# Kernel optimization log

Hardware: AMD Instinct MI355X
Metric: run time of the kernel (lower is better)

Reference implementation:

```python
import jax, jax.numpy as jnp
import numpy as np

# fp4 e2m1 representable magnitudes and round-to-nearest midpoints
_FP4_LEVELS = jnp.array([0.0, 0.5, 1.0, 1.5, 2.0, 3.0, 4.0, 6.0], dtype=jnp.float32)
_FP4_MIDS = jnp.array([0.25, 0.75, 1.25, 1.75, 2.5, 3.5, 5.0], dtype=jnp.float32)


def fp4_get_scalar(x):
    return jnp.mean(jnp.abs(x))


def fp4_quant_dequant(x, s):
    # quant(x, s) then rquant(x, s): round x/s to nearest fp4e2m1 value, scale back
    y = x / s
    idx = jnp.searchsorted(_FP4_MIDS, jnp.abs(y), side='right')
    q = jnp.sign(y) * _FP4_LEVELS[idx]
    return q * s


def setup_inputs() -> dict:
    key = jax.random.key(0)
    k1, k2, k3 = jax.random.split(key, 3)
    B, S, IN, OUT = 4, 2048, 4096, 4096
    input = jax.random.normal(k1, (B, S, IN), dtype=jnp.float32)
    # kaiming-uniform-ish weight, small bias
    bound_w = np.sqrt(6.0 / IN) / np.sqrt(1 + 5.0)
    weight = jax.random.uniform(k2, (OUT, IN), minval=-bound_w, maxval=bound_w, dtype=jnp.float32)
    bound_b = 1.0 / np.sqrt(IN)
    bias = jax.random.uniform(k3, (OUT,), minval=-bound_b, maxval=bound_b, dtype=jnp.float32)
    return {"input": input, "weight": weight, "bias": bias}


def reference(input, weight, bias):
    q_scalar = 1.0
    input_scalar = fp4_get_scalar(input) * q_scalar
    weight_scalar = fp4_get_scalar(weight) * q_scalar
    x_q = fp4_quant_dequant(input, input_scalar)      # [B,S,IN]
    w_q = fp4_quant_dequant(weight, weight_scalar)    # [OUT,IN]
    out = jnp.einsum('bsi,oi->bso', x_q, w_q) + bias  # [B,S,OUT]
    return out
```

## Files before the change

### kernel.cpp

```cpp
#include <hip/hip_runtime.h>
#include <hip/hip_bf16.h>
#include <stdint.h>

typedef __attribute__((ext_vector_type(16))) float f32x16;
typedef __attribute__((ext_vector_type(8))) int i32x8;

#define M_DIM 8192
#define N_DIM 4096
#define K_DIM 4096
#define NX_INV (1.0f / 33554432.0f)
#define NW_INV (1.0f / 16777216.0f)

#define AS3(p) ((__attribute__((address_space(3))) uint32_t*)(uint32_t)(uintptr_t)(p))
#define AS1(p) ((const __attribute__((address_space(1))) uint32_t*)(uintptr_t)(p))

__global__ void absum2_kernel(const float* __restrict__ x, const float* __restrict__ w,
                              double* __restrict__ sums) {
    bool isw = blockIdx.x >= 2048;
    const float4* src = (const float4*)(isw ? w : x);
    int n4  = isw ? (16777216 / 4) : (33554432 / 4);
    int bid = isw ? (blockIdx.x - 2048) : blockIdx.x;
    int nb  = isw ? 1024 : 2048;
    int i = bid * blockDim.x + threadIdx.x;
    int stride = nb * blockDim.x;
    float s = 0.f;
    for (; i < n4; i += stride) {
        float4 v = src[i];
        s += fabsf(v.x) + fabsf(v.y) + fabsf(v.z) + fabsf(v.w);
    }
    #pragma unroll
    for (int off = 32; off >= 1; off >>= 1) s += __shfl_down(s, off, 64);
    __shared__ float wsum[4];
    int lane = threadIdx.x & 63, wid = threadIdx.x >> 6;
    if (lane == 0) wsum[wid] = s;
    __syncthreads();
    if (threadIdx.x == 0) {
        double tot = (double)wsum[0] + (double)wsum[1] + (double)wsum[2] + (double)wsum[3];
        atomicAdd(&sums[isw ? 1 : 0], tot);
    }
}

__device__ __forceinline__ uint32_t enc_nib_t(float x, float t0, float t1, float t2,
                                              float t3, float t4, float t5, float t6) {
    float a = fabsf(x);
    uint32_t idx;
    if (a < t3) idx = (a < t1) ? ((a < t0) ? 0u : 1u) : ((a < t2) ? 2u : 3u);
    else        idx = (a < t5) ? ((a < t4) ? 4u : 5u) : ((a < t6) ? 6u : 7u);
    return idx | ((__float_as_uint(x) >> 31) << 3);
}

__global__ void quant2_kernel(const float* __restrict__ X, const float* __restrict__ W,
                              uint32_t* __restrict__ Xp, uint32_t* __restrict__ Wp,
                              const double* __restrict__ sums) {
    __shared__ float4 tile[32 * 64];

    bool isw = blockIdx.x >= 4096;
    const float* src_base = isw ? W : X;
    uint32_t* dst = isw ? Wp : Xp;
    float s = (float)(sums[isw ? 1 : 0]) * (isw ? NW_INV : NX_INV);
    int bid = isw ? (blockIdx.x - 4096) : blockIdx.x;

    float t0 = 0.25f * s, t1 = 0.75f * s, t2 = 1.25f * s, t3 = 1.75f * s;
    float t4 = 2.5f * s,  t5 = 3.5f * s,  t6 = 5.0f * s;

    int mb  = bid >> 4;
    int ktg = bid & 15;
    int t = threadIdx.x;

    {
        int row0 = t >> 6;
        int col4 = t & 63;
        const float4* src = (const float4*)(src_base + (size_t)(mb * 32 + row0) * K_DIM + ktg * 256) + col4;
        #pragma unroll
        for (int p = 0; p < 8; p++) {
            int row = p * 4 + row0;
            tile[row * 64 + (col4 ^ (row & 7))] = src[(size_t)p * 4 * (K_DIM / 4)];
        }
    }
    __syncthreads();

    int w = t >> 6;
    int l = t & 63;
    int row = l & 31;
    int ub = w * 16 + (l >> 5) * 8;
    uint32_t o[4];
    #pragma unroll
    for (int d = 0; d < 4; d++) {
        float4 f0 = tile[row * 64 + ((ub + 2 * d)     ^ (row & 7))];
        float4 f1 = tile[row * 64 + ((ub + 2 * d + 1) ^ (row & 7))];
        o[d] =  enc_nib_t(f0.x, t0,t1,t2,t3,t4,t5,t6)
             | (enc_nib_t(f0.y, t0,t1,t2,t3,t4,t5,t6) << 4)
             | (enc_nib_t(f0.z, t0,t1,t2,t3,t4,t5,t6) << 8)
             | (enc_nib_t(f0.w, t0,t1,t2,t3,t4,t5,t6) << 12)
             | (enc_nib_t(f1.x, t0,t1,t2,t3,t4,t5,t6) << 16)
             | (enc_nib_t(f1.y, t0,t1,t2,t3,t4,t5,t6) << 20)
             | (enc_nib_t(f1.z, t0,t1,t2,t3,t4,t5,t6) << 24)
             | (enc_nib_t(f1.w, t0,t1,t2,t3,t4,t5,t6) << 28);
    }
    int kt = ktg * 4 + w;
    *(uint4*)(dst + ((size_t)(mb * 64 + kt) * 64 + l) * 4) = make_uint4(o[0], o[1], o[2], o[3]);
}

#define NWG 512

__device__ __forceinline__ void glds16(const uint32_t* g, uint32_t* l) {
    __builtin_amdgcn_global_load_lds(AS1(g), AS3(l), 16, 0, 0);
}

__device__ __forceinline__ i32x8 dupfrag(uint4 u) {
    i32x8 v;
    v[0] = u.x; v[1] = u.y; v[2] = u.z; v[3] = u.w;
    v[4] = u.x; v[5] = u.y; v[6] = u.z; v[7] = u.w;
    return v;
}

#define MFMA2(VA, C0, C1) do {                                                    \
    i32x8 va_ = dupfrag(VA);                                                      \
    C0 = __builtin_amdgcn_mfma_scale_f32_32x32x64_f8f6f4(va_, vb0_, C0, 4, 4, 0, 0x7F7F7F7F, 0, 0x7F7F7F7F); \
    C1 = __builtin_amdgcn_mfma_scale_f32_32x32x64_f8f6f4(va_, vb1_, C1, 4, 4, 0, 0x7F7F7F7F, 0, 0x7F7F7F7F); \
} while (0)

#define EPI(ACC, MM, NN) do {                                                     \
    int col_ = colb + (NN) * 32;                                                  \
    float bv_ = bias[col_];                                                       \
    _Pragma("unroll")                                                             \
    for (int i = 0; i < 16; i++) {                                                \
        int row_ = rowb + (MM) * 32 + (i & 3) + ((i >> 2) << 3);                  \
        __builtin_nontemporal_store(ACC[i] * scale + bv_,                         \
                                    &C[(size_t)row_ * N_DIM + col_]);             \
    }                                                                             \
} while (0)

__global__ __launch_bounds__(512, 2)
void gemm_kernel(const uint32_t* __restrict__ Ap, const uint32_t* __restrict__ Bp,
                 const float* __restrict__ bias, float* __restrict__ C,
                 const double* __restrict__ sums) {
    __shared__ uint32_t lds[4 * 4096];

    int bid = blockIdx.x;
    int swz = (bid & 7) * 64 + (bid >> 3);
    int bm = (swz >> 4) * 256;
    int bn = (swz & 15) * 256;

    int t = threadIdx.x;
    int lane = t & 63;
    int wid = t >> 6;
    int wm = wid >> 2;
    int wn = wid & 3;

    const uint32_t* gA = Ap + (size_t)((bm >> 5) + (t >> 6)) * 16384 + (t & 63) * 4;
    const uint32_t* gB = Bp + (size_t)((bn >> 5) + (t >> 6)) * 16384 + (t & 63) * 4;
    uint32_t* ldA = lds + t * 4;
    uint32_t* ldB = lds + 2048 + t * 4;

    int oA0 = ((wm * 4 + 0) * 64 + lane) * 4;
    int oA1 = ((wm * 4 + 1) * 64 + lane) * 4;
    int oA2 = ((wm * 4 + 2) * 64 + lane) * 4;
    int oA3 = ((wm * 4 + 3) * 64 + lane) * 4;
    int oB0 = 2048 + ((wn * 2 + 0) * 64 + lane) * 4;
    int oB1 = 2048 + ((wn * 2 + 1) * 64 + lane) * 4;

    f32x16 acc00 = (f32x16)0.f, acc01 = (f32x16)0.f;
    f32x16 acc10 = (f32x16)0.f, acc11 = (f32x16)0.f;
    f32x16 acc20 = (f32x16)0.f, acc21 = (f32x16)0.f;
    f32x16 acc30 = (f32x16)0.f, acc31 = (f32x16)0.f;

    glds16(gA + 0,   ldA + 0);
    glds16(gB + 0,   ldB + 0);
    glds16(gA + 256, ldA + 4096);
    glds16(gB + 256, ldB + 4096);

    for (int kt = 0; kt < 64; kt++) {
        if (kt < 63) asm volatile("s_waitcnt vmcnt(2)" ::: "memory");
        else         asm volatile("s_waitcnt vmcnt(0)" ::: "memory");
        __builtin_amdgcn_s_barrier();

        const uint32_t* rb = lds + (kt & 3) * 4096;
        int so = ((kt + 2) & 3) * 4096;

        if (kt < 62) glds16(gA + (kt + 2) * 256, ldA + so);
        uint4 rA0 = *(const uint4*)&rb[oA0];
        uint4 rA1 = *(const uint4*)&rb[oA1];
        uint4 rB0 = *(const uint4*)&rb[oB0];
        uint4 rB1 = *(const uint4*)&rb[oB1];
        i32x8 vb0_ = dupfrag(rB0);
        i32x8 vb1_ = dupfrag(rB1);
        __builtin_amdgcn_s_setprio(1);
        MFMA2(rA0, acc00, acc01);
        MFMA2(rA1, acc10, acc11);
        __builtin_amdgcn_s_setprio(0);
        __builtin_amdgcn_s_barrier();

        if (kt < 62) glds16(gB + (kt + 2) * 256, ldB + so);
        uint4 rA2 = *(const uint4*)&rb[oA2];
        uint4 rA3 = *(const uint4*)&rb[oA3];
        __builtin_amdgcn_s_setprio(1);
        MFMA2(rA2, acc20, acc21);
        MFMA2(rA3, acc30, acc31);
        __builtin_amdgcn_s_setprio(0);
    }

    float scale = (float)((sums[0] * (1.0 / 33554432.0)) * (sums[1] * (1.0 / 16777216.0)));

    int colb = bn + wn * 64 + (lane & 31);
    int rowb = bm + wm * 128 + ((lane >> 5) << 2);
    EPI(acc00, 0, 0); EPI(acc01, 0, 1);
    EPI(acc10, 1, 0); EPI(acc11, 1, 1);
    EPI(acc20, 2, 0); EPI(acc21, 2, 1);
    EPI(acc30, 3, 0); EPI(acc31, 3, 1);
}

extern "C" void kernel_launch(void* const* d_in, const int* in_sizes, int n_in,
                              void* d_out, int out_size, void* d_ws, size_t ws_size,
                              hipStream_t stream) {
    const float* x    = (const float*)d_in[0];
    const float* w    = (const float*)d_in[1];
    const float* bias = (const float*)d_in[2];
    float* out = (float*)d_out;

    double* sums = (double*)d_ws;
    uint32_t* Xp = (uint32_t*)((char*)d_ws + 1024);
    uint32_t* Wp = Xp + (size_t)256 * 64 * 64 * 4;

    hipMemsetAsync(d_ws, 0, 1024, stream);
    absum2_kernel<<<3072, 256, 0, stream>>>(x, w, sums);
    quant2_kernel<<<6144, 256, 0, stream>>>(x, w, Xp, Wp, sums);
    gemm_kernel<<<NWG, 512, 0, stream>>>(Xp, Wp, bias, out, sums);
}
```

Baseline: 220.3 us.

## Load B fragments directly to registers, stage only A through LDS

Each wave now loads its B operand fragments straight from global memory into registers with a two-stage register double buffer, instead of staging B through LDS. Only A goes through LDS, which halves shared memory use and removes the second barrier per k-step, and the loop is unrolled by two. The cost is that the B tile is loaded redundantly by each wave row (two wm groups), so global/L2 traffic for B rises, and the vmcnt wait logic now has to account for the extra register loads.

```diff
diff --git a/kernel.cpp b/kernel.cpp
--- a/kernel.cpp
+++ b/kernel.cpp
@@ -120,6 +120,30 @@
     C1 = __builtin_amdgcn_mfma_scale_f32_32x32x64_f8f6f4(va_, vb1_, C1, 4, 4, 0, 0x7F7F7F7F, 0, 0x7F7F7F7F); \
 } while (0)
 
+#define STEP(S, KT) do {                                                          \
+    if ((KT) < 63) asm volatile("s_waitcnt vmcnt(3)" ::: "memory");               \
+    else           asm volatile("s_waitcnt vmcnt(0)" ::: "memory");               \
+    __builtin_amdgcn_s_barrier();                                                 \
+    const uint32_t* rb_ = lds + (((KT) & 3) << 11);                               \
+    i32x8 vb0_ = dupfrag(S##b0);                                                  \
+    i32x8 vb1_ = dupfrag(S##b1);                                                  \
+    if ((KT) + 2 < 64) {                                                          \
+        glds16(gA + ((KT) + 2) * 256, lds + ((((KT) + 2) & 3) << 11) + t * 4);    \
+        S##b0 = *(const uint4*)(pB0 + (size_t)((KT) + 2) * 256);                  \
+        S##b1 = *(const uint4*)(pB1 + (size_t)((KT) + 2) * 256);                  \
+    }                                                                             \
+    uint4 rA0_ = *(const uint4*)&rb_[oA0];                                        \
+    uint4 rA1_ = *(const uint4*)&rb_[oA1];                                        \
+    uint4 rA2_ = *(const uint4*)&rb_[oA2];                                        \
+    uint4 rA3_ = *(const uint4*)&rb_[oA3];                                        \
+    __builtin_amdgcn_s_setprio(1);                                                \
+    MFMA2(rA0_, acc00, acc01);                                                    \
+    MFMA2(rA1_, acc10, acc11);                                                    \
+    MFMA2(rA2_, acc20, acc21);                                                    \
+    MFMA2(rA3_, acc30, acc31);                                                    \
+    __builtin_amdgcn_s_setprio(0);                                                \
+} while (0)
+
 #define EPI(ACC, MM, NN) do {                                                     \
     int col_ = colb + (NN) * 32;                                                  \
     float bv_ = bias[col_];                                                       \
@@ -135,7 +159,7 @@
 void gemm_kernel(const uint32_t* __restrict__ Ap, const uint32_t* __restrict__ Bp,
                  const float* __restrict__ bias, float* __restrict__ C,
                  const double* __restrict__ sums) {
-    __shared__ uint32_t lds[4 * 4096];
+    __shared__ uint32_t lds[4 * 2048];
 
     int bid = blockIdx.x;
     int swz = (bid & 7) * 64 + (bid >> 3);
@@ -149,55 +173,32 @@
     int wn = wid & 3;
 
     const uint32_t* gA = Ap + (size_t)((bm >> 5) + (t >> 6)) * 16384 + (t & 63) * 4;
-    const uint32_t* gB = Bp + (size_t)((bn >> 5) + (t >> 6)) * 16384 + (t & 63) * 4;
-    uint32_t* ldA = lds + t * 4;
-    uint32_t* ldB = lds + 2048 + t * 4;
+
+    const uint32_t* pB0 = Bp + (size_t)((bn >> 5) + wn * 2 + 0) * 16384 + lane * 4;
+    const uint32_t* pB1 = Bp + (size_t)((bn >> 5) + wn * 2 + 1) * 16384 + lane * 4;
 
     int oA0 = ((wm * 4 + 0) * 64 + lane) * 4;
     int oA1 = ((wm * 4 + 1) * 64 + lane) * 4;
     int oA2 = ((wm * 4 + 2) * 64 + lane) * 4;
     int oA3 = ((wm * 4 + 3) * 64 + lane) * 4;
-    int oB0 = 2048 + ((wn * 2 + 0) * 64 + lane) * 4;
-    int oB1 = 2048 + ((wn * 2 + 1) * 64 + lane) * 4;
 
     f32x16 acc00 = (f32x16)0.f, acc01 = (f32x16)0.f;
     f32x16 acc10 = (f32x16)0.f, acc11 = (f32x16)0.f;
     f32x16 acc20 = (f32x16)0.f, acc21 = (f32x16)0.f;
     f32x16 acc30 = (f32x16)0.f, acc31 = (f32x16)0.f;
 
-    glds16(gA + 0,   ldA + 0);
-    glds16(gB + 0,   ldB + 0);
-    glds16(gA + 256, ldA + 4096);
-    glds16(gB + 256, ldB + 4096);
-
-    for (int kt = 0; kt < 64; kt++) {
-        if (kt < 63) asm volatile("s_waitcnt vmcnt(2)" ::: "memory");
-        else         asm volatile("s_waitcnt vmcnt(0)" ::: "memory");
-        __builtin_amdgcn_s_barrier();
-
-        const uint32_t* rb = lds + (kt & 3) * 4096;
-        int so = ((kt + 2) & 3) * 4096;
-
-        if (kt < 62) glds16(gA + (kt + 2) * 256, ldA + so);
-        uint4 rA0 = *(const uint4*)&rb[oA0];
-        uint4 rA1 = *(const uint4*)&rb[oA1];
-        uint4 rB0 = *(const uint4*)&rb[oB0];
-        uint4 rB1 = *(const uint4*)&rb[oB1];
-        i32x8 vb0_ = dupfrag(rB0);
-        i32x8 vb1_ = dupfrag(rB1);
-        __builtin_amdgcn_s_setprio(1);
-        MFMA2(rA0, acc00, acc01);
-        MFMA2(rA1, acc10, acc11);
-        __builtin_amdgcn_s_setprio(0);
-        __builtin_amdgcn_s_barrier();
-
-        if (kt < 62) glds16(gB + (kt + 2) * 256, ldB + so);
-        uint4 rA2 = *(const uint4*)&rb[oA2];
-        uint4 rA3 = *(const uint4*)&rb[oA3];
-        __builtin_amdgcn_s_setprio(1);
-        MFMA2(rA2, acc20, acc21);
-        MFMA2(rA3, acc30, acc31);
-        __builtin_amdgcn_s_setprio(0);
+    uint4 S0b0, S0b1, S1b0, S1b1;
+
+    glds16(gA + 0, lds + t * 4);
+    S0b0 = *(const uint4*)(pB0);
+    S0b1 = *(const uint4*)(pB1);
+    glds16(gA + 256, lds + 2048 + t * 4);
+    S1b0 = *(const uint4*)(pB0 + 256);
+    S1b1 = *(const uint4*)(pB1 + 256);
+
+    for (int kt = 0; kt < 64; kt += 2) {
+        STEP(S0, kt);
+        STEP(S1, kt + 1);
     }
 
     float scale = (float)((sums[0] * (1.0 / 33554432.0)) * (sums[1] * (1.0 / 16777216.0)));
```

Result: faster. 200.9 us (-8.8%).

## Split GEMM block into 16 waves with 64x64 warp tiles and one barrier

Applied to the files above, without the earlier changes.

The GEMM workgroup grows from 512 to 1024 threads. Each of the 16 waves now computes a 64x64 sub-tile with four accumulators instead of a 128x64 tile with eight. The A and B global-to-LDS copies merge into one load per thread per k-step, and the second mid-iteration barrier and the setprio hints are dropped. The aim is more waves to hide latency and less synchronisation. In exchange, each wave reads more LDS fragments per MFMA. The (1024,3) launch bound may also force a very low per-wave register budget, which could cause spills.

```diff
diff --git a/kernel.cpp b/kernel.cpp
--- a/kernel.cpp
+++ b/kernel.cpp
@@ -114,11 +114,8 @@
     return v;
 }
 
-#define MFMA2(VA, C0, C1) do {                                                    \
-    i32x8 va_ = dupfrag(VA);                                                      \
-    C0 = __builtin_amdgcn_mfma_scale_f32_32x32x64_f8f6f4(va_, vb0_, C0, 4, 4, 0, 0x7F7F7F7F, 0, 0x7F7F7F7F); \
-    C1 = __builtin_amdgcn_mfma_scale_f32_32x32x64_f8f6f4(va_, vb1_, C1, 4, 4, 0, 0x7F7F7F7F, 0, 0x7F7F7F7F); \
-} while (0)
+#define MFMA(VA, VB, CC) \
+    CC = __builtin_amdgcn_mfma_scale_f32_32x32x64_f8f6f4(VA, VB, CC, 4, 4, 0, 0x7F7F7F7F, 0, 0x7F7F7F7F)
 
 #define EPI(ACC, MM, NN) do {                                                     \
     int col_ = colb + (NN) * 32;                                                  \
@@ -131,7 +128,7 @@
     }                                                                             \
 } while (0)
 
-__global__ __launch_bounds__(512, 2)
+__global__ __launch_bounds__(1024, 3)
 void gemm_kernel(const uint32_t* __restrict__ Ap, const uint32_t* __restrict__ Bp,
                  const float* __restrict__ bias, float* __restrict__ C,
                  const double* __restrict__ sums) {
@@ -145,69 +142,53 @@
     int t = threadIdx.x;
     int lane = t & 63;
     int wid = t >> 6;
-    int wm = wid >> 2;
-    int wn = wid & 3;
-
-    const uint32_t* gA = Ap + (size_t)((bm >> 5) + (t >> 6)) * 16384 + (t & 63) * 4;
-    const uint32_t* gB = Bp + (size_t)((bn >> 5) + (t >> 6)) * 16384 + (t & 63) * 4;
-    uint32_t* ldA = lds + t * 4;
-    uint32_t* ldB = lds + 2048 + t * 4;
-
-    int oA0 = ((wm * 4 + 0) * 64 + lane) * 4;
-    int oA1 = ((wm * 4 + 1) * 64 + lane) * 4;
-    int oA2 = ((wm * 4 + 2) * 64 + lane) * 4;
-    int oA3 = ((wm * 4 + 3) * 64 + lane) * 4;
-    int oB0 = 2048 + ((wn * 2 + 0) * 64 + lane) * 4;
-    int oB1 = 2048 + ((wn * 2 + 1) * 64 + lane) * 4;
+    int wm4 = wid >> 2;
+    int wn4 = wid & 3;
+
+    const uint32_t* gsrc = (t < 512)
+        ? Ap + (size_t)((bm >> 5) + (t >> 6)) * 16384 + (t & 63) * 4
+        : Bp + (size_t)((bn >> 5) + ((t >> 6) - 8)) * 16384 + (t & 63) * 4;
+    int ldst = t * 4;
+
+    int oA0 = (2 * wm4 + 0) * 256 + lane * 4;
+    int oA1 = (2 * wm4 + 1) * 256 + lane * 4;
+    int oB0 = 2048 + (2 * wn4 + 0) * 256 + lane * 4;
+    int oB1 = 2048 + (2 * wn4 + 1) * 256 + lane * 4;
 
     f32x16 acc00 = (f32x16)0.f, acc01 = (f32x16)0.f;
     f32x16 acc10 = (f32x16)0.f, acc11 = (f32x16)0.f;
-    f32x16 acc20 = (f32x16)0.f, acc21 = (f32x16)0.f;
-    f32x16 acc30 = (f32x16)0.f, acc31 = (f32x16)0.f;
-
-    glds16(gA + 0,   ldA + 0);
-    glds16(gB + 0,   ldB + 0);
-    glds16(gA + 256, ldA + 4096);
-    glds16(gB + 256, ldB + 4096);
+
+    glds16(gsrc + 0,   lds + ldst);
+    glds16(gsrc + 256, lds + 4096 + ldst);
 
     for (int kt = 0; kt < 64; kt++) {
-        if (kt < 63) asm volatile("s_waitcnt vmcnt(2)" ::: "memory");
+        if (kt < 63) asm volatile("s_waitcnt vmcnt(1)" ::: "memory");
         else         asm volatile("s_waitcnt vmcnt(0)" ::: "memory");
         __builtin_amdgcn_s_barrier();
 
         const uint32_t* rb = lds + (kt & 3) * 4096;
-        int so = ((kt + 2) & 3) * 4096;
-
-        if (kt < 62) glds16(gA + (kt + 2) * 256, ldA + so);
+        if (kt < 62) glds16(gsrc + (kt + 2) * 256, lds + ((kt + 2) & 3) * 4096 + ldst);
+
         uint4 rA0 = *(const uint4*)&rb[oA0];
         uint4 rA1 = *(const uint4*)&rb[oA1];
         uint4 rB0 = *(const uint4*)&rb[oB0];
         uint4 rB1 = *(const uint4*)&rb[oB1];
-        i32x8 vb0_ = dupfrag(rB0);
-        i32x8 vb1_ = dupfrag(rB1);
-        __builtin_amdgcn_s_setprio(1);
-        MFMA2(rA0, acc00, acc01);
-        MFMA2(rA1, acc10, acc11);
-        __builtin_amdgcn_s_setprio(0);
-        __builtin_amdgcn_s_barrier();
-
-        if (kt < 62) glds16(gB + (kt + 2) * 256, ldB + so);
-        uint4 rA2 = *(const uint4*)&rb[oA2];
-        uint4 rA3 = *(const uint4*)&rb[oA3];
-        __builtin_amdgcn_s_setprio(1);
-        MFMA2(rA2, acc20, acc21);
-        MFMA2(rA3, acc30, acc31);
-        __builtin_amdgcn_s_setprio(0);
+        i32x8 vb0 = dupfrag(rB0);
+        i32x8 vb1 = dupfrag(rB1);
+        i32x8 va0 = dupfrag(rA0);
+        MFMA(va0, vb0, acc00);
+        MFMA(va0, vb1, acc01);
+        i32x8 va1 = dupfrag(rA1);
+        MFMA(va1, vb0, acc10);
+        MFMA(va1, vb1, acc11);
     }
 
     float scale = (float)((sums[0] * (1.0 / 33554432.0)) * (sums[1] * (1.0 / 16777216.0)));
 
-    int colb = bn + wn * 64 + (lane & 31);
-    int rowb = bm + wm * 128 + ((lane >> 5) << 2);
+    int colb = bn + wn4 * 64 + (lane & 31);
+    int rowb = bm + wm4 * 64 + ((lane >> 5) << 2);
     EPI(acc00, 0, 0); EPI(acc01, 0, 1);
     EPI(acc10, 1, 0); EPI(acc11, 1, 1);
-    EPI(acc20, 2, 0); EPI(acc21, 2, 1);
-    EPI(acc30, 3, 0); EPI(acc31, 3, 1);
 }
 
 extern "C" void kernel_launch(void* const* d_in, const int* in_sizes, int n_in,
@@ -225,5 +206,5 @@
     hipMemsetAsync(d_ws, 0, 1024, stream);
     absum2_kernel<<<3072, 256, 0, stream>>>(x, w, sums);
     quant2_kernel<<<6144, 256, 0, stream>>>(x, w, Xp, Wp, sums);
-    gemm_kernel<<<NWG, 512, 0, stream>>>(Xp, Wp, bias, out, sums);
-}
+    gemm_kernel<<<NWG, 1024, 0, stream>>>(Xp, Wp, bias, out, sums);
+}
```

After: 189.6 us. 1.16x faster.

## Deepen LDS prefetch to three stages and register-double-buffer MFMA fragments

Applied to the files above, without the earlier changes.

The K loop is restructured so global-to-LDS prefetch runs three tiles ahead instead of two. Each iteration loads the next tile's A/B fragments from LDS into registers while the MFMAs consume the fragments loaded in the previous iteration. This cuts the loop to one barrier per iteration instead of two and removes the s_setprio toggling, with the aim of hiding LDS read latency behind matrix work. The cost is extra VGPRs for the second set of fragments, which could hurt register pressure or occupancy at 512 threads with two blocks per SM.

```diff
diff --git a/kernel.cpp b/kernel.cpp
--- a/kernel.cpp
+++ b/kernel.cpp
@@ -114,11 +114,8 @@
     return v;
 }
 
-#define MFMA2(VA, C0, C1) do {                                                    \
-    i32x8 va_ = dupfrag(VA);                                                      \
-    C0 = __builtin_amdgcn_mfma_scale_f32_32x32x64_f8f6f4(va_, vb0_, C0, 4, 4, 0, 0x7F7F7F7F, 0, 0x7F7F7F7F); \
-    C1 = __builtin_amdgcn_mfma_scale_f32_32x32x64_f8f6f4(va_, vb1_, C1, 4, 4, 0, 0x7F7F7F7F, 0, 0x7F7F7F7F); \
-} while (0)
+#define MFMA(VA, VB, CC) \
+    CC = __builtin_amdgcn_mfma_scale_f32_32x32x64_f8f6f4(VA, VB, CC, 4, 4, 0, 0x7F7F7F7F, 0, 0x7F7F7F7F)
 
 #define EPI(ACC, MM, NN) do {                                                     \
     int col_ = colb + (NN) * 32;                                                  \
@@ -150,8 +147,6 @@
 
     const uint32_t* gA = Ap + (size_t)((bm >> 5) + (t >> 6)) * 16384 + (t & 63) * 4;
     const uint32_t* gB = Bp + (size_t)((bn >> 5) + (t >> 6)) * 16384 + (t & 63) * 4;
-    uint32_t* ldA = lds + t * 4;
-    uint32_t* ldB = lds + 2048 + t * 4;
 
     int oA0 = ((wm * 4 + 0) * 64 + lane) * 4;
     int oA1 = ((wm * 4 + 1) * 64 + lane) * 4;
@@ -165,39 +160,57 @@
     f32x16 acc20 = (f32x16)0.f, acc21 = (f32x16)0.f;
     f32x16 acc30 = (f32x16)0.f, acc31 = (f32x16)0.f;
 
-    glds16(gA + 0,   ldA + 0);
-    glds16(gB + 0,   ldB + 0);
-    glds16(gA + 256, ldA + 4096);
-    glds16(gB + 256, ldB + 4096);
+    uint4 Fa0, Fa1, Fa2, Fa3, Fb0, Fb1;
+    i32x8 Da0, Da1, Da2, Da3, Db0, Db1;
+
+    #pragma unroll
+    for (int pt = 0; pt < 3; pt++) {
+        glds16(gA + pt * 256, lds + pt * 4096 + t * 4);
+        glds16(gB + pt * 256, lds + pt * 4096 + 2048 + t * 4);
+    }
+    asm volatile("s_waitcnt vmcnt(4)" ::: "memory");
+    __builtin_amdgcn_s_barrier();
+    Fa0 = *(const uint4*)&lds[oA0];
+    Fa1 = *(const uint4*)&lds[oA1];
+    Fa2 = *(const uint4*)&lds[oA2];
+    Fa3 = *(const uint4*)&lds[oA3];
+    Fb0 = *(const uint4*)&lds[oB0];
+    Fb1 = *(const uint4*)&lds[oB1];
+    Db0 = dupfrag(Fb0); Db1 = dupfrag(Fb1);
+    Da0 = dupfrag(Fa0); Da1 = dupfrag(Fa1);
+    Da2 = dupfrag(Fa2); Da3 = dupfrag(Fa3);
 
     for (int kt = 0; kt < 64; kt++) {
-        if (kt < 63) asm volatile("s_waitcnt vmcnt(2)" ::: "memory");
-        else         asm volatile("s_waitcnt vmcnt(0)" ::: "memory");
-        __builtin_amdgcn_s_barrier();
-
-        const uint32_t* rb = lds + (kt & 3) * 4096;
-        int so = ((kt + 2) & 3) * 4096;
-
-        if (kt < 62) glds16(gA + (kt + 2) * 256, ldA + so);
-        uint4 rA0 = *(const uint4*)&rb[oA0];
-        uint4 rA1 = *(const uint4*)&rb[oA1];
-        uint4 rB0 = *(const uint4*)&rb[oB0];
-        uint4 rB1 = *(const uint4*)&rb[oB1];
-        i32x8 vb0_ = dupfrag(rB0);
-        i32x8 vb1_ = dupfrag(rB1);
-        __builtin_amdgcn_s_setprio(1);
-        MFMA2(rA0, acc00, acc01);
-        MFMA2(rA1, acc10, acc11);
-        __builtin_amdgcn_s_setprio(0);
-        __builtin_amdgcn_s_barrier();
-
-        if (kt < 62) glds16(gB + (kt + 2) * 256, ldB + so);
-        uint4 rA2 = *(const uint4*)&rb[oA2];
-        uint4 rA3 = *(const uint4*)&rb[oA3];
-        __builtin_amdgcn_s_setprio(1);
-        MFMA2(rA2, acc20, acc21);
-        MFMA2(rA3, acc30, acc31);
-        __builtin_amdgcn_s_setprio(0);
+        if (kt < 62)       asm volatile("s_waitcnt vmcnt(2)" ::: "memory");
+        else if (kt == 62) asm volatile("s_waitcnt vmcnt(0)" ::: "memory");
+        if (kt < 63) __builtin_amdgcn_s_barrier();
+
+        if (kt < 61) {
+            int so = ((kt + 3) & 3) * 4096;
+            glds16(gA + (kt + 3) * 256, lds + so + t * 4);
+            glds16(gB + (kt + 3) * 256, lds + so + 2048 + t * 4);
+        }
+
+        if (kt < 63) {
+            const uint32_t* rb = lds + ((kt + 1) & 3) * 4096;
+            Fa0 = *(const uint4*)&rb[oA0];
+            Fa1 = *(const uint4*)&rb[oA1];
+            Fa2 = *(const uint4*)&rb[oA2];
+            Fa3 = *(const uint4*)&rb[oA3];
+            Fb0 = *(const uint4*)&rb[oB0];
+            Fb1 = *(const uint4*)&rb[oB1];
+        }
+
+        MFMA(Da0, Db0, acc00); MFMA(Da0, Db1, acc01);
+        MFMA(Da1, Db0, acc10); MFMA(Da1, Db1, acc11);
+        MFMA(Da2, Db0, acc20); MFMA(Da2, Db1, acc21);
+        MFMA(Da3, Db0, acc30); MFMA(Da3, Db1, acc31);
+
+        if (kt < 63) {
+            Db0 = dupfrag(Fb0); Db1 = dupfrag(Fb1);
+            Da0 = dupfrag(Fa0); Da1 = dupfrag(Fa1);
+            Da2 = dupfrag(Fa2); Da3 = dupfrag(Fa3);
+        }
     }
 
     float scale = (float)((sums[0] * (1.0 / 33554432.0)) * (sums[1] * (1.0 / 16777216.0)));
```

Result: faster. 202.1 us (-8.2%).
